# Performance work log

Hardware: AMD Instinct MI355X
Metric: run time of the kernel (lower is better)

The kernel has to match this reference:

```python
import jax, jax.numpy as jnp
import numpy as np
import math

NEG_INF = -10000.0

def setup_inputs() -> dict:
    key = jax.random.key(0)
    k1, k2, k3 = jax.random.split(key, 3)
    B, Sq, Sk, H, D = 2, 2048, 2048, 16, 64
    q = jax.random.normal(k1, (B, Sq, H, D), dtype=jnp.float32)
    kv = jax.random.normal(k2, (B, Sk, 2, H, D), dtype=jnp.float32)
    key_padding_mask = jax.random.randint(k3, (B, Sk), 0, 2).astype(jnp.bool_)
    return {"q": q, "kv": kv, "key_padding_mask": key_padding_mask}

def reference(q, kv, key_padding_mask):
    # q: (B, Sq, H, D); kv: (B, Sk, 2, H, D); key_padding_mask: (B, Sk) True=keep
    D = q.shape[-1]
    softmax_scale = 1.0 / math.sqrt(D)
    k = kv[:, :, 0]  # (B, Sk, H, D)
    v = kv[:, :, 1]  # (B, Sk, H, D)
    # (B, H, Sq, Sk) score matrix
    scores = jnp.einsum('bthd,bshd->bhts', q, k * softmax_scale)
    # additive padding mask: 0 where keep, NEG_INF where masked out
    pad = jnp.where(key_padding_mask, 0.0, NEG_INF).astype(scores.dtype)
    scores = scores + pad[:, None, None, :]
    attention = jax.nn.softmax(scores, axis=-1)
    # dropout_p = 0.0 (eval mode) -> no-op
    output = jnp.einsum('bhts,bshd->bthd', attention, v)
    return output
```

## Files before the change

### kernel.cpp

```cpp
#include <hip/hip_runtime.h>

typedef unsigned short u16;
typedef unsigned int   u32;
typedef u16   u16x8 __attribute__((ext_vector_type(8)));
typedef float f32x4 __attribute__((ext_vector_type(4)));
typedef __bf16 bf16x8 __attribute__((ext_vector_type(8)));
typedef u32   u32x2 __attribute__((ext_vector_type(2)));
typedef u32   u32x4 __attribute__((ext_vector_type(4)));

#define QSCALE  0.18033688011112f
#define BM_OPEN  -28.8539008177793f
#define BM_MASK  -14455.8043097f

__device__ __forceinline__ u16 f2bf(float x){
  __bf16 h = (__bf16)x;
  return __builtin_bit_cast(u16, h);
}
__device__ __forceinline__ f32x4 mfma16x16x32(u16x8 a, u16x8 b, f32x4 c){
  return __builtin_amdgcn_mfma_f32_16x16x32_bf16(
      __builtin_bit_cast(bf16x8, a), __builtin_bit_cast(bf16x8, b), c, 0, 0, 0);
}
__device__ __forceinline__ void gld16(const void* g, void* l){
  __builtin_amdgcn_global_load_lds(
      (const __attribute__((address_space(1))) u32*)g,
      (__attribute__((address_space(3))) u32*)l, 16, 0, 0);
}


__global__ __launch_bounds__(256, 4)
void prepass(const float* __restrict__ KV, const int* __restrict__ MASK,
             u16* __restrict__ IMG, float* __restrict__ BIASM)
{
  const int tid = threadIdx.x;
  const int bid = blockIdx.x;
  const int kt = bid & 31;
  const int h  = (bid >> 5) & 15;
  const int b  = bid >> 9;
  const int kb = kt*64;
  const size_t kv_b = (size_t)b*(2048u*2048u);
  u16* tile = IMG + (size_t)bid * 8192;

  {
    const int skey = tid >> 2, scp = tid & 3;
    const float* kp = KV + kv_b + (size_t)(kb + skey)*2048 + h*64 + 16*scp;
    f32x4 f0 = *(const f32x4*)(kp);
    f32x4 f1 = *(const f32x4*)(kp + 4);
    f32x4 f2 = *(const f32x4*)(kp + 8);
    f32x4 f3 = *(const f32x4*)(kp + 12);
    u16x8 c0, c1;
    #pragma unroll
    for (int e = 0; e < 4; ++e){
      c0[e] = f2bf(f0[e]); c0[e+4] = f2bf(f1[e]);
      c1[e] = f2bf(f2[e]); c1[e+4] = f2bf(f3[e]);
    }
    const int idx0 = skey*64 + (((2*scp) ^ (skey & 7)) << 3);
    *(u16x8*)&tile[idx0]     = c0;
    *(u16x8*)&tile[idx0 ^ 8] = c1;
  }
  {
    const int sdb = tid & 7, ssp = tid >> 3;
    const float* vp = KV + kv_b + (size_t)(kb + 2*ssp)*2048 + 1024 + h*64 + 8*sdb;
    f32x4 r0a = *(const f32x4*)(vp);
    f32x4 r0b = *(const f32x4*)(vp + 4);
    f32x4 r1a = *(const f32x4*)(vp + 2048);
    f32x4 r1b = *(const f32x4*)(vp + 2048 + 4);
    u32* vimg = (u32*)(tile + 4096);
    const int wc = ssp >> 2, wi = ssp & 3;
    #pragma unroll
    for (int j = 0; j < 4; ++j){
      const int d0 = 8*sdb + j;
      const int d1 = d0 + 4;
      vimg[d0*32 + ((wc ^ (d0 & 7)) << 2) + wi] = (u32)f2bf(r0a[j]) | ((u32)f2bf(r1a[j]) << 16);
      vimg[d1*32 + ((wc ^ (d1 & 7)) << 2) + wi] = (u32)f2bf(r0b[j]) | ((u32)f2bf(r1b[j]) << 16);
    }
  }
  if (h == 0 && tid < 64){
    const int s = kb + tid;
    BIASM[b*2048 + s] = MASK[b*2048 + s] ? BM_OPEN : BM_MASK;
  }
}

template<int PRE>
__global__ __launch_bounds__(256, 2)
void attn_main(const float* __restrict__ Q, const float* __restrict__ KV,
               const int* __restrict__ MASK, const u16* __restrict__ IMG,
               const float* __restrict__ BIASM, float* __restrict__ OUT)
{
  __shared__ __align__(16) u16 KVbuf[3][8192];
  __shared__ __align__(16) u32 Pw[4][32*36];
  __shared__ __align__(16) float BiasLds[2048];

  const int tid  = threadIdx.x;
  const int w    = tid >> 6;
  const int lane = tid & 63;
  const int lg   = lane >> 4;
  const int ln   = lane & 15;

  const int bid0 = blockIdx.x;
  const int bid  = (bid0 & 7)*64 + (bid0 >> 3);
  const int qt  = bid & 15;
  const int h   = (bid >> 4) & 15;
  const int b   = bid >> 8;

  const int qbase = qt*128 + w*32;
  const size_t q_b  = (size_t)b * (2048u*1024u);
  const size_t kv_b = (size_t)b * (2048u*2048u);

  const int lnoff = ln*64;
  const int ck0   = ((lg ^ (ln & 7)) << 3);
  const int ck1   = ck0 ^ 32;

  u16x8 Qf[2][2];
  #pragma unroll
  for (int G = 0; G < 2; ++G){
    const int qrow = qbase + 16*G + ln;
    const float* qp = Q + q_b + (size_t)qrow*1024 + h*64 + 8*lg;
    #pragma unroll
    for (int kc = 0; kc < 2; ++kc){
      f32x4 a = *(const f32x4*)(qp + 32*kc);
      f32x4 c = *(const f32x4*)(qp + 32*kc + 4);
      u16x8 v;
      #pragma unroll
      for (int e = 0; e < 4; ++e){
        v[e]     = f2bf(a[e] * QSCALE);
        v[e + 4] = f2bf(c[e] * QSCALE);
      }
      Qf[G][kc] = v;
    }
  }

  f32x4 Oacc[2][4];
  #pragma unroll
  for (int G = 0; G < 2; ++G)
    #pragma unroll
    for (int dt = 0; dt < 4; ++dt)
      Oacc[G][dt] = f32x4{0.f,0.f,0.f,0.f};
  float lrun[2] = { 0.f, 0.f };

  const char* img0 = (const char*)IMG + (size_t)((b*16 + h)*32) * 16384;
  const int so = tid*16;
  const int skey = tid >> 2, scp = tid & 3;
  const int sdb  = tid & 7,  ssp = tid >> 3;
  const float* kp0 = KV + kv_b + (size_t)skey*2048 + h*64 + 16*scp;
  const float* vp0 = KV + kv_b + (size_t)(2*ssp)*2048 + 1024 + h*64 + 8*sdb;
  f32x4 kf0, kf1, kf2, kf3, va, vb2, vc, vd;

#define STAGE_ISSUE(T, DST) do{                                               \
    const char* g_ = img0 + (size_t)(T)*16384;                                \
    char* l_ = (char*)(DST);                                                  \
    gld16(g_+so,        l_+so);                                               \
    gld16(g_+so+4096,   l_+so+4096);                                          \
    gld16(g_+so+8192,   l_+so+8192);                                          \
    gld16(g_+so+12288,  l_+so+12288);                                         \
  }while(0)

#define BIAS_STAGE() do{                                                      \
    const char* gb_ = (const char*)BIASM + (size_t)b*8192;                    \
    char* lb_ = (char*)BiasLds;                                               \
    gld16(gb_+so,      lb_+so);                                               \
    gld16(gb_+so+4096, lb_+so+4096);                                          \
  }while(0)

#define STAGE_REG(T) do{                                                      \
    const float* kp_ = kp0 + (size_t)(T)*64*2048;                             \
    kf0=*(const f32x4*)(kp_);   kf1=*(const f32x4*)(kp_+4);                   \
    kf2=*(const f32x4*)(kp_+8); kf3=*(const f32x4*)(kp_+12);                  \
    const float* vp_ = vp0 + (size_t)(T)*64*2048;                             \
    va=*(const f32x4*)(vp_);      vb2=*(const f32x4*)(vp_+4);                 \
    vc=*(const f32x4*)(vp_+2048); vd =*(const f32x4*)(vp_+2048+4);            \
  }while(0)

#define STAGE_WRITE(DST) do{                                                  \
    u16x8 c0_, c1_;                                                           \
    _Pragma("unroll") for (int e_=0; e_<4; ++e_){                             \
      c0_[e_]=f2bf(kf0[e_]); c0_[e_+4]=f2bf(kf1[e_]);                         \
      c1_[e_]=f2bf(kf2[e_]); c1_[e_+4]=f2bf(kf3[e_]); }                       \
    const int kix_ = skey*64 + (((2*scp) ^ (skey & 7)) << 3);                 \
    *(u16x8*)&(DST)[kix_]     = c0_;                                          \
    *(u16x8*)&(DST)[kix_ ^ 8] = c1_;                                          \
    u32* vimg_ = (u32*)((DST)+4096);                                          \
    const int wc_ = ssp >> 2, wi_ = ssp & 3;                                  \
    _Pragma("unroll") for (int j_=0; j_<4; ++j_){                             \
      const int d0_=8*sdb+j_, d1_=d0_+4;                                      \
      vimg_[d0_*32 + ((wc_ ^ (d0_&7)) << 2) + wi_] = (u32)f2bf(va[j_])  | ((u32)f2bf(vc[j_])<<16); \
      vimg_[d1_*32 + ((wc_ ^ (d1_&7)) << 2) + wi_] = (u32)f2bf(vb2[j_]) | ((u32)f2bf(vd[j_])<<16); \
    }                                                                         \
  }while(0)

#define COMPUTE(T, CUR) do{                                                   \
    const u16* Kb_ = (CUR);                                                   \
    const u16* Vb_ = (CUR) + 4096;                                            \
    f32x4 S[2][4];                                                            \
    _Pragma("unroll") for (int ct = 0; ct < 4; ++ct){                         \
      f32x4 bv;                                                               \
      if constexpr (PRE){                                                     \
        bv = *(const f32x4*)&BiasLds[(T)*64 + 16*ct + 4*lg];                  \
      } else {                                                                \
        const int4 mv = *(const int4*)(MASK + b*2048 + (T)*64 + 16*ct + 4*lg);\
        bv[0] = mv.x ? BM_OPEN : BM_MASK;                                     \
        bv[1] = mv.y ? BM_OPEN : BM_MASK;                                     \
        bv[2] = mv.z ? BM_OPEN : BM_MASK;                                     \
        bv[3] = mv.w ? BM_OPEN : BM_MASK;                                     \
      }                                                                       \
      S[0][ct] = bv;                                                          \
      S[1][ct] = bv;                                                          \
    }                                                                         \
    __builtin_amdgcn_s_setprio(1);                                            \
    _Pragma("unroll") for (int ct = 0; ct < 4; ++ct){                         \
      const int rb = ct*1024 + lnoff;                                         \
      u16x8 k0 = *(const u16x8*)&Kb_[rb + ck0];                               \
      u16x8 k1 = *(const u16x8*)&Kb_[rb + ck1];                               \
      S[0][ct] = mfma16x16x32(k0, Qf[0][0], S[0][ct]);                        \
      S[1][ct] = mfma16x16x32(k0, Qf[1][0], S[1][ct]);                        \
      S[0][ct] = mfma16x16x32(k1, Qf[0][1], S[0][ct]);                        \
      S[1][ct] = mfma16x16x32(k1, Qf[1][1], S[1][ct]);                        \
    }                                                                         \
    __builtin_amdgcn_s_setprio(0);                                            \
    _Pragma("unroll") for (int G = 0; G < 2; ++G){                            \
      float ps = 0.f;                                                         \
      _Pragma("unroll") for (int ct = 0; ct < 4; ++ct){                       \
        _Pragma("unroll") for (int r = 0; r < 4; ++r){                        \
          const float p = __builtin_amdgcn_exp2f(S[G][ct][r]);                \
          S[G][ct][r] = p;                                                    \
          ps += p;                                                            \
        }                                                                     \
      }                                                                       \
      lrun[G] += ps;                                                          \
      _Pragma("unroll") for (int ct = 0; ct < 4; ++ct){                       \
        u32x2 pw;                                                             \
        pw[0] = (u32)f2bf(S[G][ct][0]) | ((u32)f2bf(S[G][ct][1]) << 16);      \
        pw[1] = (u32)f2bf(S[G][ct][2]) | ((u32)f2bf(S[G][ct][3]) << 16);      \
        *(u32x2*)&Pw[w][(16*G + ln)*36 + 8*ct + 2*lg] = pw;                   \
      }                                                                       \
    }                                                                         \
    asm volatile("" ::: "memory");                                            \
    u16x8 Pf[2][2];                                                           \
    _Pragma("unroll") for (int G = 0; G < 2; ++G)                             \
      _Pragma("unroll") for (int sc = 0; sc < 2; ++sc){                       \
        u32x4 pr = *(const u32x4*)&Pw[w][(16*G + ln)*36 + 4*lg + 16*sc];      \
        Pf[G][sc] = __builtin_bit_cast(u16x8, pr);                            \
      }                                                                       \
    __builtin_amdgcn_s_setprio(1);                                            \
    _Pragma("unroll") for (int dt = 0; dt < 4; ++dt){                         \
      const int rb = dt*1024 + lnoff;                                         \
      u16x8 v0 = *(const u16x8*)&Vb_[rb + ck0];                               \
      u16x8 v1 = *(const u16x8*)&Vb_[rb + ck1];                               \
      Oacc[0][dt] = mfma16x16x32(v0, Pf[0][0], Oacc[0][dt]);                  \
      Oacc[1][dt] = mfma16x16x32(v0, Pf[1][0], Oacc[1][dt]);                  \
      Oacc[0][dt] = mfma16x16x32(v1, Pf[0][1], Oacc[0][dt]);                  \
      Oacc[1][dt] = mfma16x16x32(v1, Pf[1][1], Oacc[1][dt]);                  \
    }                                                                         \
    __builtin_amdgcn_s_setprio(0);                                            \
  }while(0)

#define SEAM(N) do{                                                           \
    __builtin_amdgcn_sched_barrier(0);                                        \
    asm volatile("s_waitcnt vmcnt(%0)" :: "i"(N) : "memory");                 \
    __builtin_amdgcn_sched_barrier(0);                                        \
    __builtin_amdgcn_s_barrier();                                             \
  }while(0)

#define PITER(T, CUR, FREE) do{                                               \
    if ((T) + 2 <= 31) STAGE_ISSUE((T)+2, FREE);                              \
    COMPUTE(T, CUR);                                                          \
    SEAM(4);                                                                  \
  }while(0)

  if constexpr (PRE){
    u16* b0 = &KVbuf[0][0];
    u16* b1 = &KVbuf[1][0];
    u16* b2 = &KVbuf[2][0];
    BIAS_STAGE();
    STAGE_ISSUE(0, b0);
    STAGE_ISSUE(1, b1);
    SEAM(4);
    for (int u = 0; u < 10; ++u){
      PITER(3*u    , b0, b2);
      PITER(3*u + 1, b1, b0);
      PITER(3*u + 2, b2, b1);
    }
    COMPUTE(30, b0);
    SEAM(0);
    COMPUTE(31, b1);
  } else {
    STAGE_REG(0);
    STAGE_WRITE(&KVbuf[0][0]);
    __syncthreads();
    for (int t = 0; t < 32; ++t){
      if (t < 31) STAGE_REG(t+1);
      COMPUTE(t, &KVbuf[t & 1][0]);
      if (t < 31){
        STAGE_WRITE(&KVbuf[(t+1) & 1][0]);
        __syncthreads();
      }
    }
  }

  #pragma unroll
  for (int G = 0; G < 2; ++G){
    float l_ = lrun[G];
    l_ += __shfl_xor(l_, 16, 64);
    l_ += __shfl_xor(l_, 32, 64);
    const float inv = 1.f / l_;
    const int qrow = qbase + 16*G + ln;
    float* op = OUT + q_b + (size_t)qrow*1024 + h*64;
    #pragma unroll
    for (int dt = 0; dt < 4; ++dt){
      f32x4 ov;
      ov[0] = Oacc[G][dt][0] * inv;
      ov[1] = Oacc[G][dt][1] * inv;
      ov[2] = Oacc[G][dt][2] * inv;
      ov[3] = Oacc[G][dt][3] * inv;
      *(f32x4*)(op + 16*dt + 4*lg) = ov;
    }
  }
#undef STAGE_ISSUE
#undef BIAS_STAGE
#undef STAGE_REG
#undef STAGE_WRITE
#undef COMPUTE
#undef SEAM
#undef PITER
}

extern "C" void kernel_launch(void* const* d_in, const int* in_sizes, int n_in,
                              void* d_out, int out_size, void* d_ws, size_t ws_size,
                              hipStream_t stream)
{
  const float* Q  = nullptr;
  const float* KV = nullptr;
  const int*   M  = nullptr;
  for (int i = 0; i < n_in; ++i){
    if      (in_sizes[i] == 4194304) Q  = (const float*)d_in[i];
    else if (in_sizes[i] == 8388608) KV = (const float*)d_in[i];
    else if (in_sizes[i] == 4096)    M  = (const int*)d_in[i];
  }
  if (!Q)  Q  = (const float*)d_in[0];
  if (!KV) KV = (const float*)d_in[1];
  if (!M)  M  = (const int*)d_in[2];
  float* O = (float*)d_out;

  const size_t NEED = 16384ull + 1024ull*16384ull;
  if (ws_size >= NEED){
    float* biasm = (float*)d_ws;
    u16*   img   = (u16*)((char*)d_ws + 16384);
    prepass<<<dim3(1024), dim3(256), 0, stream>>>(KV, M, img, biasm);
    attn_main<1><<<dim3(512), dim3(256), 0, stream>>>(Q, KV, M, img, biasm, O);
  } else {
    attn_main<0><<<dim3(512), dim3(256), 0, stream>>>(Q, KV, M, nullptr, nullptr, O);
  }
}
```

Measured before the change: 66.43 us.

## Switch to 32x32x16 MFMA and keep P in registers via permlane swaps

Replaces the 16x16x32 bf16 MFMA tiling with 32x32x16 MFMAs, so each wave handles 32 query rows as one tile and issues fewer, larger matrix instructions. The softmax probabilities are packed with v_cvt_pk_bf16_f32 and rearranged across lane halves with v_permlane32_swap, so the P operand for the PV product is built in registers. This removes the per-wave LDS round trip through the Pw buffer. The trade-off is larger accumulator register tiles and reliance on gfx950-specific instructions whose lane mapping must match exactly.

```diff
diff --git a/kernel.cpp b/kernel.cpp
--- a/kernel.cpp
+++ b/kernel.cpp
@@ -4,8 +4,8 @@
 typedef unsigned int   u32;
 typedef u16   u16x8 __attribute__((ext_vector_type(8)));
 typedef float f32x4 __attribute__((ext_vector_type(4)));
+typedef float f32x16 __attribute__((ext_vector_type(16)));
 typedef __bf16 bf16x8 __attribute__((ext_vector_type(8)));
-typedef u32   u32x2 __attribute__((ext_vector_type(2)));
 typedef u32   u32x4 __attribute__((ext_vector_type(4)));
 
 #define QSCALE  0.18033688011112f
@@ -16,14 +16,22 @@
   __bf16 h = (__bf16)x;
   return __builtin_bit_cast(u16, h);
 }
-__device__ __forceinline__ f32x4 mfma16x16x32(u16x8 a, u16x8 b, f32x4 c){
-  return __builtin_amdgcn_mfma_f32_16x16x32_bf16(
+__device__ __forceinline__ f32x16 mfma32(u16x8 a, u16x8 b, f32x16 c){
+  return __builtin_amdgcn_mfma_f32_32x32x16_bf16(
       __builtin_bit_cast(bf16x8, a), __builtin_bit_cast(bf16x8, b), c, 0, 0, 0);
 }
 __device__ __forceinline__ void gld16(const void* g, void* l){
   __builtin_amdgcn_global_load_lds(
       (const __attribute__((address_space(1))) u32*)g,
       (__attribute__((address_space(3))) u32*)l, 16, 0, 0);
+}
+__device__ __forceinline__ u32 cvtpk(float lo, float hi){
+  u32 d;
+  asm("v_cvt_pk_bf16_f32 %0, %1, %2" : "=v"(d) : "v"(lo), "v"(hi));
+  return d;
+}
+__device__ __forceinline__ void plswap(u32 &x, u32 &y){
+  asm("v_permlane32_swap_b32 %0, %1" : "+v"(x), "+v"(y));
 }
 
 
@@ -87,14 +95,13 @@
                const float* __restrict__ BIASM, float* __restrict__ OUT)
 {
   __shared__ __align__(16) u16 KVbuf[3][8192];
-  __shared__ __align__(16) u32 Pw[4][32*36];
   __shared__ __align__(16) float BiasLds[2048];
 
   const int tid  = threadIdx.x;
   const int w    = tid >> 6;
   const int lane = tid & 63;
-  const int lg   = lane >> 4;
-  const int ln   = lane & 15;
+  const int hi   = lane >> 5;
+  const int lq   = lane & 31;
 
   const int bid0 = blockIdx.x;
   const int bid  = (bid0 & 7)*64 + (bid0 >> 3);
@@ -106,36 +113,32 @@
   const size_t q_b  = (size_t)b * (2048u*1024u);
   const size_t kv_b = (size_t)b * (2048u*2048u);
 
-  const int lnoff = ln*64;
-  const int ck0   = ((lg ^ (ln & 7)) << 3);
-  const int ck1   = ck0 ^ 32;
-
-  u16x8 Qf[2][2];
-  #pragma unroll
-  for (int G = 0; G < 2; ++G){
-    const int qrow = qbase + 16*G + ln;
-    const float* qp = Q + q_b + (size_t)qrow*1024 + h*64 + 8*lg;
-    #pragma unroll
-    for (int kc = 0; kc < 2; ++kc){
-      f32x4 a = *(const f32x4*)(qp + 32*kc);
-      f32x4 c = *(const f32x4*)(qp + 32*kc + 4);
+  const int sw7 = lq & 7;
+
+  u16x8 Qf[4];
+  {
+    const int qrow = qbase + lq;
+    const float* qp = Q + q_b + (size_t)qrow*1024 + h*64 + 8*hi;
+    #pragma unroll
+    for (int kc = 0; kc < 4; ++kc){
+      f32x4 a = *(const f32x4*)(qp + 16*kc);
+      f32x4 c = *(const f32x4*)(qp + 16*kc + 4);
       u16x8 v;
       #pragma unroll
       for (int e = 0; e < 4; ++e){
         v[e]     = f2bf(a[e] * QSCALE);
         v[e + 4] = f2bf(c[e] * QSCALE);
       }
-      Qf[G][kc] = v;
-    }
-  }
-
-  f32x4 Oacc[2][4];
+      Qf[kc] = v;
+    }
+  }
+
+  f32x16 Oa[2];
   #pragma unroll
-  for (int G = 0; G < 2; ++G)
-    #pragma unroll
-    for (int dt = 0; dt < 4; ++dt)
-      Oacc[G][dt] = f32x4{0.f,0.f,0.f,0.f};
-  float lrun[2] = { 0.f, 0.f };
+  for (int dt = 0; dt < 2; ++dt)
+    #pragma unroll
+    for (int r = 0; r < 16; ++r) Oa[dt][r] = 0.f;
+  float lrun = 0.f;
 
   const char* img0 = (const char*)IMG + (size_t)((b*16 + h)*32) * 16384;
   const int so = tid*16;
@@ -189,66 +192,62 @@
 
 #define COMPUTE(T, CUR) do{                                                   \
     const u16* Kb_ = (CUR);                                                   \
-    const u16* Vb_ = (CUR) + 4096;                                            \
-    f32x4 S[2][4];                                                            \
-    _Pragma("unroll") for (int ct = 0; ct < 4; ++ct){                         \
-      f32x4 bv;                                                               \
-      if constexpr (PRE){                                                     \
-        bv = *(const f32x4*)&BiasLds[(T)*64 + 16*ct + 4*lg];                  \
-      } else {                                                                \
-        const int4 mv = *(const int4*)(MASK + b*2048 + (T)*64 + 16*ct + 4*lg);\
-        bv[0] = mv.x ? BM_OPEN : BM_MASK;                                     \
-        bv[1] = mv.y ? BM_OPEN : BM_MASK;                                     \
-        bv[2] = mv.z ? BM_OPEN : BM_MASK;                                     \
-        bv[3] = mv.w ? BM_OPEN : BM_MASK;                                     \
+    const u32* vimg_ = (const u32*)((CUR) + 4096);                            \
+    f32x16 S[2];                                                              \
+    _Pragma("unroll") for (int ct = 0; ct < 2; ++ct){                         \
+      _Pragma("unroll") for (int m = 0; m < 4; ++m){                          \
+        f32x4 bq;                                                             \
+        if constexpr (PRE){                                                   \
+          bq = *(const f32x4*)&BiasLds[(T)*64 + 32*ct + 8*m + 4*hi];          \
+        } else {                                                              \
+          const int4 mv = *(const int4*)(MASK + b*2048 + (T)*64 + 32*ct + 8*m + 4*hi); \
+          bq[0] = mv.x ? BM_OPEN : BM_MASK;                                   \
+          bq[1] = mv.y ? BM_OPEN : BM_MASK;                                   \
+          bq[2] = mv.z ? BM_OPEN : BM_MASK;                                   \
+          bq[3] = mv.w ? BM_OPEN : BM_MASK;                                   \
+        }                                                                     \
+        S[ct][4*m+0] = bq[0]; S[ct][4*m+1] = bq[1];                           \
+        S[ct][4*m+2] = bq[2]; S[ct][4*m+3] = bq[3];                           \
       }                                                                       \
-      S[0][ct] = bv;                                                          \
-      S[1][ct] = bv;                                                          \
     }                                                                         \
     __builtin_amdgcn_s_setprio(1);                                            \
-    _Pragma("unroll") for (int ct = 0; ct < 4; ++ct){                         \
-      const int rb = ct*1024 + lnoff;                                         \
-      u16x8 k0 = *(const u16x8*)&Kb_[rb + ck0];                               \
-      u16x8 k1 = *(const u16x8*)&Kb_[rb + ck1];                               \
-      S[0][ct] = mfma16x16x32(k0, Qf[0][0], S[0][ct]);                        \
-      S[1][ct] = mfma16x16x32(k0, Qf[1][0], S[1][ct]);                        \
-      S[0][ct] = mfma16x16x32(k1, Qf[0][1], S[0][ct]);                        \
-      S[1][ct] = mfma16x16x32(k1, Qf[1][1], S[1][ct]);                        \
+    _Pragma("unroll") for (int ct = 0; ct < 2; ++ct){                         \
+      _Pragma("unroll") for (int kc = 0; kc < 4; ++kc){                       \
+        u16x8 kf = *(const u16x8*)&Kb_[(32*ct + lq)*64 + (((2*kc + hi) ^ sw7) << 3)]; \
+        S[ct] = mfma32(kf, Qf[kc], S[ct]);                                    \
+      }                                                                       \
     }                                                                         \
     __builtin_amdgcn_s_setprio(0);                                            \
-    _Pragma("unroll") for (int G = 0; G < 2; ++G){                            \
-      float ps = 0.f;                                                         \
-      _Pragma("unroll") for (int ct = 0; ct < 4; ++ct){                       \
-        _Pragma("unroll") for (int r = 0; r < 4; ++r){                        \
-          const float p = __builtin_amdgcn_exp2f(S[G][ct][r]);                \
-          S[G][ct][r] = p;                                                    \
-          ps += p;                                                            \
-        }                                                                     \
+    u32 pa[2][4], pb[2][4];                                                   \
+    float ps = 0.f;                                                           \
+    _Pragma("unroll") for (int ct = 0; ct < 2; ++ct){                         \
+      _Pragma("unroll") for (int m = 0; m < 4; ++m){                          \
+        const float p0 = __builtin_amdgcn_exp2f(S[ct][4*m+0]);                \
+        const float p1 = __builtin_amdgcn_exp2f(S[ct][4*m+1]);                \
+        const float p2 = __builtin_amdgcn_exp2f(S[ct][4*m+2]);                \
+        const float p3 = __builtin_amdgcn_exp2f(S[ct][4*m+3]);                \
+        ps += (p0 + p1) + (p2 + p3);                                          \
+        pa[ct][m] = cvtpk(p0, p1);                                            \
+        pb[ct][m] = cvtpk(p2, p3);                                            \
       }                                                                       \
-      lrun[G] += ps;                                                          \
-      _Pragma("unroll") for (int ct = 0; ct < 4; ++ct){                       \
-        u32x2 pw;                                                             \
-        pw[0] = (u32)f2bf(S[G][ct][0]) | ((u32)f2bf(S[G][ct][1]) << 16);      \
-        pw[1] = (u32)f2bf(S[G][ct][2]) | ((u32)f2bf(S[G][ct][3]) << 16);      \
-        *(u32x2*)&Pw[w][(16*G + ln)*36 + 8*ct + 2*lg] = pw;                   \
+    }                                                                         \
+    lrun += ps;                                                               \
+               \
+    u16x8 Pf[4];                                                              \
+    _Pragma("unroll") for (int ct = 0; ct < 2; ++ct){                         \
+      plswap(pa[ct][0], pa[ct][1]);  plswap(pb[ct][0], pb[ct][1]);            \
+      plswap(pa[ct][2], pa[ct][3]);  plswap(pb[ct][2], pb[ct][3]);            \
+      u32x4 f0_ = { pa[ct][0], pb[ct][0], pa[ct][1], pb[ct][1] };             \
+      u32x4 f1_ = { pa[ct][2], pb[ct][2], pa[ct][3], pb[ct][3] };             \
+      Pf[2*ct+0] = __builtin_bit_cast(u16x8, f0_);                            \
+      Pf[2*ct+1] = __builtin_bit_cast(u16x8, f1_);                            \
+    }                                                                         \
+    __builtin_amdgcn_s_setprio(1);                                            \
+    _Pragma("unroll") for (int dt = 0; dt < 2; ++dt){                         \
+      _Pragma("unroll") for (int sc = 0; sc < 4; ++sc){                       \
+        u32x4 vv = *(const u32x4*)&vimg_[(32*dt + lq)*32 + (((2*sc + hi) ^ sw7) << 2)]; \
+        Oa[dt] = mfma32(__builtin_bit_cast(u16x8, vv), Pf[sc], Oa[dt]);       \
       }                                                                       \
-    }                                                                         \
-    asm volatile("" ::: "memory");                                            \
-    u16x8 Pf[2][2];                                                           \
-    _Pragma("unroll") for (int G = 0; G < 2; ++G)                             \
-      _Pragma("unroll") for (int sc = 0; sc < 2; ++sc){                       \
-        u32x4 pr = *(const u32x4*)&Pw[w][(16*G + ln)*36 + 4*lg + 16*sc];      \
-        Pf[G][sc] = __builtin_bit_cast(u16x8, pr);                            \
-      }                                                                       \
-    __builtin_amdgcn_s_setprio(1);                                            \
-    _Pragma("unroll") for (int dt = 0; dt < 4; ++dt){                         \
-      const int rb = dt*1024 + lnoff;                                         \
-      u16x8 v0 = *(const u16x8*)&Vb_[rb + ck0];                               \
-      u16x8 v1 = *(const u16x8*)&Vb_[rb + ck1];                               \
-      Oacc[0][dt] = mfma16x16x32(v0, Pf[0][0], Oacc[0][dt]);                  \
-      Oacc[1][dt] = mfma16x16x32(v0, Pf[1][0], Oacc[1][dt]);                  \
-      Oacc[0][dt] = mfma16x16x32(v1, Pf[0][1], Oacc[0][dt]);                  \
-      Oacc[1][dt] = mfma16x16x32(v1, Pf[1][1], Oacc[1][dt]);                  \
     }                                                                         \
     __builtin_amdgcn_s_setprio(0);                                            \
   }while(0)
@@ -296,22 +295,22 @@
     }
   }
 
-  #pragma unroll
-  for (int G = 0; G < 2; ++G){
-    float l_ = lrun[G];
-    l_ += __shfl_xor(l_, 16, 64);
-    l_ += __shfl_xor(l_, 32, 64);
+  {
+    float l_ = lrun + __shfl_xor(lrun, 32, 64);
     const float inv = 1.f / l_;
-    const int qrow = qbase + 16*G + ln;
+    const int qrow = qbase + lq;
     float* op = OUT + q_b + (size_t)qrow*1024 + h*64;
     #pragma unroll
-    for (int dt = 0; dt < 4; ++dt){
-      f32x4 ov;
-      ov[0] = Oacc[G][dt][0] * inv;
-      ov[1] = Oacc[G][dt][1] * inv;
-      ov[2] = Oacc[G][dt][2] * inv;
-      ov[3] = Oacc[G][dt][3] * inv;
-      *(f32x4*)(op + 16*dt + 4*lg) = ov;
+    for (int dt = 0; dt < 2; ++dt){
+      #pragma unroll
+      for (int m = 0; m < 4; ++m){
+        f32x4 ov;
+        ov[0] = Oa[dt][4*m+0] * inv;
+        ov[1] = Oa[dt][4*m+1] * inv;
+        ov[2] = Oa[dt][4*m+2] * inv;
+        ov[3] = Oa[dt][4*m+3] * inv;
+        *(f32x4*)(op + 32*dt + 8*m + 4*hi) = ov;
+      }
     }
   }
 #undef STAGE_ISSUE
```

Result: faster. 59.91 us (-9.8%).
